# Optimization experiments

Measured on AMD Instinct MI355X. Metric: run time of the kernel, lower is better.

## Reference

```python
import jax, jax.numpy as jnp
import numpy as np

NUM_ITERATIONS = 10
NUM_NODES = 16


def setup_inputs() -> dict:
    key = jax.random.key(0)
    v = jax.random.uniform(key, (131072, NUM_NODES * NUM_NODES), dtype=jnp.float32)
    return {"v": v}


def reference(v) -> jnp.ndarray:
    batch_size = v.shape[0]
    # S = reshape(b, n, n) then transpose last two dims
    S = v.reshape((batch_size, NUM_NODES, NUM_NODES)).transpose(0, 2, 1)
    S = S + 1e-6
    for _ in range(NUM_ITERATIONS):
        # torch: solve against diag(colsums) -> divide each column by its sum
        S = S / jnp.sum(S, axis=1, keepdims=True)
        # torch: solve against diag(rowsums) -> divide each row by its sum
        S = S / jnp.sum(S, axis=2, keepdims=True)
    return S
```

## Files before the change

### kernel.cpp

```cpp
#include <hip/hip_runtime.h>


#define NITER 10

template <int CTRL>
__device__ __forceinline__ float dpp_add(float x) {
    int xi = __builtin_bit_cast(int, x);
    int yi = __builtin_amdgcn_update_dpp(xi, xi, CTRL, 0xF, 0xF, false);
    return x + __builtin_bit_cast(float, yi);
}

__global__ __launch_bounds__(256) void sinkhorn16_kernel(
        const float* __restrict__ v, float* __restrict__ out, int nmat) {
    const int tid = blockIdx.x * 256 + threadIdx.x;
    const int b   = tid >> 4;
    if (b >= nmat) return;
    const int idx = tid & 15;
    const int r   = idx & 3;
    const int c   = idx >> 2;

    const float* base = v + (size_t)b * 256 + c * 64 + r * 4;
    float4 fj[4];
    fj[0] = *(const float4*)(base +  0);
    fj[1] = *(const float4*)(base + 16);
    fj[2] = *(const float4*)(base + 32);
    fj[3] = *(const float4*)(base + 48);

    float blk[4][4];
#pragma unroll
    for (int j = 0; j < 4; ++j) {
        blk[0][j] = fj[j].x + 1e-6f;
        blk[1][j] = fj[j].y + 1e-6f;
        blk[2][j] = fj[j].z + 1e-6f;
        blk[3][j] = fj[j].w + 1e-6f;
    }

#pragma unroll
    for (int it = 0; it < NITER; ++it) {
        float cs[4];
#pragma unroll
        for (int j = 0; j < 4; ++j) {
            cs[j] = (blk[0][j] + blk[1][j]) + (blk[2][j] + blk[3][j]);
            cs[j] = dpp_add<0xB1>(cs[j]);
            cs[j] = dpp_add<0x4E>(cs[j]);
            const float rc = __builtin_amdgcn_rcpf(cs[j]);
#pragma unroll
            for (int i = 0; i < 4; ++i) blk[i][j] *= rc;
        }
#pragma unroll
        for (int i = 0; i < 4; ++i) {
            float rs = (blk[i][0] + blk[i][1]) + (blk[i][2] + blk[i][3]);
            rs = dpp_add<0x124>(rs);
            rs = dpp_add<0x128>(rs);
            const float rr = __builtin_amdgcn_rcpf(rs);
#pragma unroll
            for (int j = 0; j < 4; ++j) blk[i][j] *= rr;
        }
    }

    float* ob = out + (size_t)b * 256 + r * 64 + c * 4;
#pragma unroll
    for (int i = 0; i < 4; ++i) {
        *(float4*)(ob + 16 * i) =
            make_float4(blk[i][0], blk[i][1], blk[i][2], blk[i][3]);
    }
}

extern "C" void kernel_launch(void* const* d_in, const int* in_sizes, int n_in,
                              void* d_out, int out_size, void* d_ws, size_t ws_size,
                              hipStream_t stream) {
    const float* v = (const float*)d_in[0];
    float* out = (float*)d_out;
    const int nmat = in_sizes[0] / 256;
    const int total_threads = nmat * 16;
    const int block = 256;
    const int grid = (total_threads + block - 1) / block;
    sinkhorn16_kernel<<<grid, block, 0, stream>>>(v, out, nmat);
}
```

Measured before the change: 234.5 us.

## Factor Sinkhorn into row/column scaling vectors with packed FP32 math, 4 threads per matrix

Rewrites the Sinkhorn iteration so the matrix stays fixed and only per-row and per-column scaling vectors are updated, applying them once at the end. Each matrix now uses 4 threads holding 4 columns each instead of 16 threads holding 4x4 blocks. The inner products use two-wide float vectors so the compiler can emit packed FP32 instructions, and only row sums need cross-lane DPP reductions. This removes the repeated full-matrix rescaling and half the shuffles, but raises registers per thread (64 values plus scales), cuts thread count fourfold, and changes load/store patterns, which may hurt occupancy and coalescing.

```diff
diff --git a/kernel.cpp b/kernel.cpp
--- a/kernel.cpp
+++ b/kernel.cpp
@@ -2,6 +2,7 @@
 
 
 #define NITER 10
+typedef float v2f __attribute__((ext_vector_type(2)));
 
 template <int CTRL>
 __device__ __forceinline__ float dpp_add(float x) {
@@ -10,59 +11,67 @@
     return x + __builtin_bit_cast(float, yi);
 }
 
+__device__ __forceinline__ float qsum(float x) {
+    x = dpp_add<0xB1>(x);
+    x = dpp_add<0x4E>(x);
+    return x;
+}
+
 __global__ __launch_bounds__(256) void sinkhorn16_kernel(
         const float* __restrict__ v, float* __restrict__ out, int nmat) {
     const int tid = blockIdx.x * 256 + threadIdx.x;
-    const int b   = tid >> 4;
+    const int b   = tid >> 2;
     if (b >= nmat) return;
-    const int idx = tid & 15;
-    const int r   = idx & 3;
-    const int c   = idx >> 2;
+    const int c   = tid & 3;
 
-    const float* base = v + (size_t)b * 256 + c * 64 + r * 4;
-    float4 fj[4];
-    fj[0] = *(const float4*)(base +  0);
-    fj[1] = *(const float4*)(base + 16);
-    fj[2] = *(const float4*)(base + 32);
-    fj[3] = *(const float4*)(base + 48);
-
-    float blk[4][4];
+    const float* base = v + (size_t)b * 256 + c * 64;
+    v2f col[4][8];
 #pragma unroll
     for (int j = 0; j < 4; ++j) {
-        blk[0][j] = fj[j].x + 1e-6f;
-        blk[1][j] = fj[j].y + 1e-6f;
-        blk[2][j] = fj[j].z + 1e-6f;
-        blk[3][j] = fj[j].w + 1e-6f;
+#pragma unroll
+        for (int g = 0; g < 4; ++g) {
+            float4 f = *(const float4*)(base + j * 16 + g * 4);
+            col[j][2 * g]     = (v2f){f.x + 1e-6f, f.y + 1e-6f};
+            col[j][2 * g + 1] = (v2f){f.z + 1e-6f, f.w + 1e-6f};
+        }
     }
+
+    v2f rv[8];
+#pragma unroll
+    for (int i2 = 0; i2 < 8; ++i2) rv[i2] = (v2f){1.0f, 1.0f};
+    float cj[4];
 
 #pragma unroll
     for (int it = 0; it < NITER; ++it) {
-        float cs[4];
 #pragma unroll
         for (int j = 0; j < 4; ++j) {
-            cs[j] = (blk[0][j] + blk[1][j]) + (blk[2][j] + blk[3][j]);
-            cs[j] = dpp_add<0xB1>(cs[j]);
-            cs[j] = dpp_add<0x4E>(cs[j]);
-            const float rc = __builtin_amdgcn_rcpf(cs[j]);
+            v2f acc = col[j][0] * rv[0];
 #pragma unroll
-            for (int i = 0; i < 4; ++i) blk[i][j] *= rc;
+            for (int i2 = 1; i2 < 8; ++i2) acc += col[j][i2] * rv[i2];
+            cj[j] = __builtin_amdgcn_rcpf(acc.x + acc.y);
         }
 #pragma unroll
-        for (int i = 0; i < 4; ++i) {
-            float rs = (blk[i][0] + blk[i][1]) + (blk[i][2] + blk[i][3]);
-            rs = dpp_add<0x124>(rs);
-            rs = dpp_add<0x128>(rs);
-            const float rr = __builtin_amdgcn_rcpf(rs);
-#pragma unroll
-            for (int j = 0; j < 4; ++j) blk[i][j] *= rr;
+        for (int i2 = 0; i2 < 8; ++i2) {
+            v2f p =  col[0][i2] * (v2f){cj[0], cj[0]};
+            p     += col[1][i2] * (v2f){cj[1], cj[1]};
+            p     += col[2][i2] * (v2f){cj[2], cj[2]};
+            p     += col[3][i2] * (v2f){cj[3], cj[3]};
+            rv[i2].x = __builtin_amdgcn_rcpf(qsum(p.x));
+            rv[i2].y = __builtin_amdgcn_rcpf(qsum(p.y));
         }
     }
 
-    float* ob = out + (size_t)b * 256 + r * 64 + c * 4;
+    float* ob = out + (size_t)b * 256 + c * 4;
 #pragma unroll
-    for (int i = 0; i < 4; ++i) {
-        *(float4*)(ob + 16 * i) =
-            make_float4(blk[i][0], blk[i][1], blk[i][2], blk[i][3]);
+    for (int i2 = 0; i2 < 8; ++i2) {
+        v2f s0 = col[0][i2] * rv[i2];
+        v2f s1 = col[1][i2] * rv[i2];
+        v2f s2 = col[2][i2] * rv[i2];
+        v2f s3 = col[3][i2] * rv[i2];
+        *(float4*)(ob + (2 * i2) * 16) =
+            make_float4(s0.x * cj[0], s1.x * cj[1], s2.x * cj[2], s3.x * cj[3]);
+        *(float4*)(ob + (2 * i2 + 1) * 16) =
+            make_float4(s0.y * cj[0], s1.y * cj[1], s2.y * cj[2], s3.y * cj[3]);
     }
 }
 
@@ -71,8 +80,8 @@
                               hipStream_t stream) {
     const float* v = (const float*)d_in[0];
     float* out = (float*)d_out;
-    const int nmat = in_sizes[0] / 256;
-    const int total_threads = nmat * 16;
+    const int nmat = in_sizes[0] >> 8;
+    const int total_threads = nmat * 4;
     const int block = 256;
     const int grid = (total_threads + block - 1) / block;
     sinkhorn16_kernel<<<grid, block, 0, stream>>>(v, out, nmat);
```

After: 240.3 us. +2.5%, slower.

## Track Sinkhorn row/column scale vectors instead of rescaling the matrix each iteration

Applied to the files above, without the earlier changes.

Rewrites the Sinkhorn loop as a diagonal-scaling formulation. The matrix stays fixed and only per-row and per-column reciprocal scale vectors are updated, with the full normalization applied once at the final store. Sums use packed 2-wide float vector math so the compiler can emit packed FMA/mul instructions. This removes the 32 per-iteration elementwise multiplies per thread, but the reordered floating-point operations may differ slightly in rounding.

```diff
diff --git a/kernel.cpp b/kernel.cpp
--- a/kernel.cpp
+++ b/kernel.cpp
@@ -2,6 +2,7 @@
 
 
 #define NITER 10
+typedef float v2f __attribute__((ext_vector_type(2)));
 
 template <int CTRL>
 __device__ __forceinline__ float dpp_add(float x) {
@@ -21,48 +22,49 @@
 
     const float* base = v + (size_t)b * 256 + c * 64 + r * 4;
     float4 fj[4];
-    fj[0] = *(const float4*)(base +  0);
-    fj[1] = *(const float4*)(base + 16);
-    fj[2] = *(const float4*)(base + 32);
-    fj[3] = *(const float4*)(base + 48);
+#pragma unroll
+    for (int j = 0; j < 4; ++j) fj[j] = *(const float4*)(base + 16 * j);
 
-    float blk[4][4];
+    v2f bp[4][2];
 #pragma unroll
-    for (int j = 0; j < 4; ++j) {
-        blk[0][j] = fj[j].x + 1e-6f;
-        blk[1][j] = fj[j].y + 1e-6f;
-        blk[2][j] = fj[j].z + 1e-6f;
-        blk[3][j] = fj[j].w + 1e-6f;
+    for (int j2 = 0; j2 < 2; ++j2) {
+        const float4 fa = fj[2 * j2], fb = fj[2 * j2 + 1];
+        bp[0][j2] = (v2f){fa.x + 1e-6f, fb.x + 1e-6f};
+        bp[1][j2] = (v2f){fa.y + 1e-6f, fb.y + 1e-6f};
+        bp[2][j2] = (v2f){fa.z + 1e-6f, fb.z + 1e-6f};
+        bp[3][j2] = (v2f){fa.w + 1e-6f, fb.w + 1e-6f};
     }
+
+    float rv[4] = {1.0f, 1.0f, 1.0f, 1.0f};
+    v2f cjp[2];
 
 #pragma unroll
     for (int it = 0; it < NITER; ++it) {
-        float cs[4];
 #pragma unroll
-        for (int j = 0; j < 4; ++j) {
-            cs[j] = (blk[0][j] + blk[1][j]) + (blk[2][j] + blk[3][j]);
-            cs[j] = dpp_add<0xB1>(cs[j]);
-            cs[j] = dpp_add<0x4E>(cs[j]);
-            const float rc = __builtin_amdgcn_rcpf(cs[j]);
-#pragma unroll
-            for (int i = 0; i < 4; ++i) blk[i][j] *= rc;
+        for (int j2 = 0; j2 < 2; ++j2) {
+            v2f acc = bp[0][j2] * (v2f){rv[0], rv[0]};
+            acc += bp[1][j2] * (v2f){rv[1], rv[1]};
+            acc += bp[2][j2] * (v2f){rv[2], rv[2]};
+            acc += bp[3][j2] * (v2f){rv[3], rv[3]};
+            float s0 = dpp_add<0x4E>(dpp_add<0xB1>(acc.x));
+            float s1 = dpp_add<0x4E>(dpp_add<0xB1>(acc.y));
+            cjp[j2] = (v2f){__builtin_amdgcn_rcpf(s0), __builtin_amdgcn_rcpf(s1)};
         }
 #pragma unroll
         for (int i = 0; i < 4; ++i) {
-            float rs = (blk[i][0] + blk[i][1]) + (blk[i][2] + blk[i][3]);
-            rs = dpp_add<0x124>(rs);
-            rs = dpp_add<0x128>(rs);
-            const float rr = __builtin_amdgcn_rcpf(rs);
-#pragma unroll
-            for (int j = 0; j < 4; ++j) blk[i][j] *= rr;
+            v2f t = bp[i][0] * cjp[0] + bp[i][1] * cjp[1];
+            float s = dpp_add<0x128>(dpp_add<0x124>(t.x + t.y));
+            rv[i] = __builtin_amdgcn_rcpf(s);
         }
     }
 
     float* ob = out + (size_t)b * 256 + r * 64 + c * 4;
 #pragma unroll
     for (int i = 0; i < 4; ++i) {
-        *(float4*)(ob + 16 * i) =
-            make_float4(blk[i][0], blk[i][1], blk[i][2], blk[i][3]);
+        const v2f rvp = (v2f){rv[i], rv[i]};
+        const v2f s0 = bp[i][0] * cjp[0] * rvp;
+        const v2f s1 = bp[i][1] * cjp[1] * rvp;
+        *(float4*)(ob + 16 * i) = make_float4(s0.x, s0.y, s1.x, s1.y);
     }
 }
 
@@ -71,7 +73,7 @@
                               hipStream_t stream) {
     const float* v = (const float*)d_in[0];
     float* out = (float*)d_out;
-    const int nmat = in_sizes[0] / 256;
+    const int nmat = in_sizes[0] >> 8;
     const int total_threads = nmat * 16;
     const int block = 256;
     const int grid = (total_threads + block - 1) / block;
```

After: 231.0 us. No clear change (-1.5%).

## Track Sinkhorn scaling vectors and process two matrices per thread with packed math

Applied to the files above, without the earlier changes.

Rewrites the Sinkhorn loop to keep the original matrix fixed and iterate only on row and column scaling vectors, applying them once at output. Each thread group now handles two matrices at once, using 2-wide float vectors so the compiler can emit packed FP32 multiply/FMA instructions. This halves the thread count and replaces per-element rescaling with dot-product style FMAs. The cost is more registers per thread, and the kernel assumes an even matrix count, since an odd trailing matrix would be dropped.

```diff
diff --git a/kernel.cpp b/kernel.cpp
--- a/kernel.cpp
+++ b/kernel.cpp
@@ -2,6 +2,7 @@
 
 
 #define NITER 10
+typedef float v2f __attribute__((ext_vector_type(2)));
 
 template <int CTRL>
 __device__ __forceinline__ float dpp_add(float x) {
@@ -10,59 +11,75 @@
     return x + __builtin_bit_cast(float, yi);
 }
 
+__device__ __forceinline__ v2f quad_allreduce(v2f a) {
+    a.x = dpp_add<0x4E>(dpp_add<0xB1>(a.x));
+    a.y = dpp_add<0x4E>(dpp_add<0xB1>(a.y));
+    return a;
+}
+__device__ __forceinline__ v2f row_allreduce(v2f a) {
+    a.x = dpp_add<0x128>(dpp_add<0x124>(a.x));
+    a.y = dpp_add<0x128>(dpp_add<0x124>(a.y));
+    return a;
+}
+__device__ __forceinline__ v2f rcp2(v2f a) {
+    return (v2f){__builtin_amdgcn_rcpf(a.x), __builtin_amdgcn_rcpf(a.y)};
+}
+
 __global__ __launch_bounds__(256) void sinkhorn16_kernel(
-        const float* __restrict__ v, float* __restrict__ out, int nmat) {
-    const int tid = blockIdx.x * 256 + threadIdx.x;
-    const int b   = tid >> 4;
-    if (b >= nmat) return;
+        const float* __restrict__ v, float* __restrict__ out, int npair) {
+    const int tid  = blockIdx.x * 256 + threadIdx.x;
+    const int pair = tid >> 4;
+    if (pair >= npair) return;
     const int idx = tid & 15;
     const int r   = idx & 3;
     const int c   = idx >> 2;
 
-    const float* base = v + (size_t)b * 256 + c * 64 + r * 4;
-    float4 fj[4];
-    fj[0] = *(const float4*)(base +  0);
-    fj[1] = *(const float4*)(base + 16);
-    fj[2] = *(const float4*)(base + 32);
-    fj[3] = *(const float4*)(base + 48);
+    const float* baseA = v + (size_t)pair * 512 + c * 64 + r * 4;
 
-    float blk[4][4];
+    v2f bp[4][4];
 #pragma unroll
     for (int j = 0; j < 4; ++j) {
-        blk[0][j] = fj[j].x + 1e-6f;
-        blk[1][j] = fj[j].y + 1e-6f;
-        blk[2][j] = fj[j].z + 1e-6f;
-        blk[3][j] = fj[j].w + 1e-6f;
+        const float4 fa = *(const float4*)(baseA + 16 * j);
+        const float4 fb = *(const float4*)(baseA + 256 + 16 * j);
+        bp[0][j] = (v2f){fa.x + 1e-6f, fb.x + 1e-6f};
+        bp[1][j] = (v2f){fa.y + 1e-6f, fb.y + 1e-6f};
+        bp[2][j] = (v2f){fa.z + 1e-6f, fb.z + 1e-6f};
+        bp[3][j] = (v2f){fa.w + 1e-6f, fb.w + 1e-6f};
     }
+
+    v2f rv[4], cj[4];
+#pragma unroll
+    for (int i = 0; i < 4; ++i) rv[i] = (v2f){1.0f, 1.0f};
 
 #pragma unroll
     for (int it = 0; it < NITER; ++it) {
-        float cs[4];
 #pragma unroll
         for (int j = 0; j < 4; ++j) {
-            cs[j] = (blk[0][j] + blk[1][j]) + (blk[2][j] + blk[3][j]);
-            cs[j] = dpp_add<0xB1>(cs[j]);
-            cs[j] = dpp_add<0x4E>(cs[j]);
-            const float rc = __builtin_amdgcn_rcpf(cs[j]);
-#pragma unroll
-            for (int i = 0; i < 4; ++i) blk[i][j] *= rc;
+            v2f acc = bp[0][j] * rv[0];
+            acc += bp[1][j] * rv[1];
+            acc += bp[2][j] * rv[2];
+            acc += bp[3][j] * rv[3];
+            cj[j] = rcp2(quad_allreduce(acc));
         }
 #pragma unroll
         for (int i = 0; i < 4; ++i) {
-            float rs = (blk[i][0] + blk[i][1]) + (blk[i][2] + blk[i][3]);
-            rs = dpp_add<0x124>(rs);
-            rs = dpp_add<0x128>(rs);
-            const float rr = __builtin_amdgcn_rcpf(rs);
-#pragma unroll
-            for (int j = 0; j < 4; ++j) blk[i][j] *= rr;
+            v2f t = bp[i][0] * cj[0];
+            t += bp[i][1] * cj[1];
+            t += bp[i][2] * cj[2];
+            t += bp[i][3] * cj[3];
+            rv[i] = rcp2(row_allreduce(t));
         }
     }
 
-    float* ob = out + (size_t)b * 256 + r * 64 + c * 4;
+    float* obA = out + (size_t)pair * 512 + r * 64 + c * 4;
 #pragma unroll
     for (int i = 0; i < 4; ++i) {
-        *(float4*)(ob + 16 * i) =
-            make_float4(blk[i][0], blk[i][1], blk[i][2], blk[i][3]);
+        const v2f s0 = bp[i][0] * cj[0] * rv[i];
+        const v2f s1 = bp[i][1] * cj[1] * rv[i];
+        const v2f s2 = bp[i][2] * cj[2] * rv[i];
+        const v2f s3 = bp[i][3] * cj[3] * rv[i];
+        *(float4*)(obA + 16 * i)       = make_float4(s0.x, s1.x, s2.x, s3.x);
+        *(float4*)(obA + 256 + 16 * i) = make_float4(s0.y, s1.y, s2.y, s3.y);
     }
 }
 
@@ -71,9 +88,10 @@
                               hipStream_t stream) {
     const float* v = (const float*)d_in[0];
     float* out = (float*)d_out;
-    const int nmat = in_sizes[0] / 256;
-    const int total_threads = nmat * 16;
+    const int nmat  = in_sizes[0] >> 8;
+    const int npair = nmat >> 1;
+    const int total_threads = npair * 16;
     const int block = 256;
     const int grid = (total_threads + block - 1) / block;
-    sinkhorn16_kernel<<<grid, block, 0, stream>>>(v, out, nmat);
+    sinkhorn16_kernel<<<grid, block, 0, stream>>>(v, out, npair);
 }
```

Result: no change. 237.6 us (+1.3%).
